# Kernel optimization log

Hardware: AMD Instinct MI355X
Metric: run time of the kernel (lower is better)

## Reference

```python
import jax, jax.numpy as jnp
import numpy as np

HIDDEN = 300
DEPTH = 3
MAX_NB = 10
AFEAT = 82
BFEAT = 6
B, N, M = 16, 2048, 4096


def setup_inputs() -> dict:
    key = jax.random.key(0)
    ks = jax.random.split(key, 16)
    s = 0.05
    return {
        "input_atom": jax.random.normal(ks[0], (B, N, AFEAT), jnp.float32),
        "input_bond": jax.random.normal(ks[1], (B, M, BFEAT), jnp.float32),
        "node_mask": jnp.ones((B, N, 1), jnp.float32),
        "atom_graph": jax.random.randint(ks[2], (B, N, MAX_NB), 0, N, jnp.int32),
        "bond_graph": jax.random.randint(ks[3], (B, N, MAX_NB), 0, M, jnp.int32),
        "num_nbs": jax.random.randint(ks[4], (B, N), 0, MAX_NB, jnp.int32),
        "W_af": jax.random.normal(ks[5], (AFEAT, HIDDEN), jnp.float32) * s,
        "W_na": jax.random.normal(ks[6], (HIDDEN, HIDDEN), jnp.float32) * s,
        "W_nb": jax.random.normal(ks[7], (BFEAT, HIDDEN), jnp.float32) * s,
        "W_sa": jax.random.normal(ks[8], (HIDDEN, HIDDEN), jnp.float32) * s,
        "W_u2": jax.random.normal(ks[9], (HIDDEN + BFEAT, HIDDEN), jnp.float32) * s,
        "b_u2": jnp.zeros((HIDDEN,), jnp.float32),
        "W_u1": jax.random.normal(ks[10], (2 * HIDDEN, HIDDEN), jnp.float32) * s,
        "b_u1": jnp.zeros((HIDDEN,), jnp.float32),
        "W_out": jax.random.normal(ks[11], (HIDDEN, 1), jnp.float32) * s,
        "b_out": jnp.zeros((1,), jnp.float32),
    }


def _wln(input_atom, input_bond, node_mask, atom_graph, bond_graph, num_nbs,
         W_af, W_na, W_nb, W_sa, W_u2, b_u2, W_u1, b_u1):
    bidx = jnp.arange(input_atom.shape[0])[:, None, None]  # (B,1,1)
    atom_feat = jax.nn.relu(input_atom @ W_af)             # (B,N,H)
    fbond_nei = input_bond[bidx, bond_graph]               # (B,N,max_nb,6) gather
    h_nei_bond = fbond_nei @ W_nb                          # constant over depth
    # neighbor validity mask from num_nbs (sequence mask)
    nb_mask = (jnp.arange(MAX_NB)[None, None, :] < num_nbs[..., None]
               ).astype(atom_feat.dtype)[..., None]        # (B,N,max_nb,1)
    kernel = None
    for _ in range(DEPTH):
        fatom_nei = atom_feat[bidx, atom_graph]            # (B,N,max_nb,H) gather
        h_nei = (fatom_nei @ W_na) * h_nei_bond
        f_nei = jnp.sum(h_nei * nb_mask, axis=-2)          # (B,N,H)
        f_self = atom_feat @ W_sa
        kernel = f_nei * f_self * node_mask                # last-layer WLN kernel
        l_nei = jnp.concatenate([fatom_nei, fbond_nei], axis=-1)
        pre_label = jax.nn.relu(l_nei @ W_u2 + b_u2)
        nei_label = jnp.sum(pre_label * nb_mask, axis=-2)
        new_label = jnp.concatenate([atom_feat, nei_label], axis=-1)
        atom_feat = jax.nn.relu(new_label @ W_u1 + b_u1)
    return kernel


def reference(input_atom, input_bond, node_mask, atom_graph, bond_graph, num_nbs,
              W_af, W_na, W_nb, W_sa, W_u2, b_u2, W_u1, b_u1, W_out, b_out):
    x = _wln(input_atom, input_bond, node_mask, atom_graph, bond_graph, num_nbs,
             W_af, W_na, W_nb, W_sa, W_u2, b_u2, W_u1, b_u1)  # (B,N,H)
    x = jnp.sum(x, axis=-2)                                   # sum pooling -> (B,H)
    return x @ W_out + b_out                                  # (B,1)
```

## Files before the change

kernel.cpp:

```cpp
#include <hip/hip_runtime.h>
#include <math.h>


typedef unsigned short ushort_t;
typedef __attribute__((ext_vector_type(8))) short bf16x8;
typedef __attribute__((ext_vector_type(8))) unsigned short ushort8;
typedef __attribute__((ext_vector_type(4))) float f32x4;

static constexpr int Hh  = 300;
static constexpr int Hp  = 320;
static constexpr int Bn  = 16;
static constexpr int Nn  = 2048;
static constexpr int Rn  = Bn * Nn;
static constexpr int NBn = 10;

__device__ __forceinline__ ushort_t f2bf(float x) {
    union { float f; unsigned u; } c; c.f = x;
    unsigned r = c.u + 0x7FFFu + ((c.u >> 16) & 1u);
    return (ushort_t)(r >> 16);
}
__device__ __forceinline__ float bf2f(ushort_t h) {
    union { float f; unsigned u; } c; c.u = ((unsigned)h) << 16;
    return c.f;
}

template<bool RELU, bool BIAS, bool CONCAT>
__global__ __launch_bounds__(256)
void mfma_gemm_k(const ushort_t* __restrict__ A, const ushort_t* __restrict__ A2,
                 int lda, int KP,
                 const ushort_t* __restrict__ Wt,
                 const float* __restrict__ bias,
                 ushort_t* __restrict__ C)
{
    __shared__ __attribute__((aligned(16))) ushort_t As[256 * 40];
    __shared__ __attribute__((aligned(16))) ushort_t Bs[64 * 40];

    const int t   = threadIdx.x;
    const int wv  = t >> 6;
    const int ln  = t & 63;
    const int lrow = ln & 15;
    const int lgrp = ln >> 4;
    const int rowBase = blockIdx.y * 256;
    const int nBase   = blockIdx.x * 64;

    f32x4 acc[4][4];
#pragma unroll
    for (int i = 0; i < 4; i++)
#pragma unroll
        for (int j = 0; j < 4; j++) acc[i][j] = (f32x4){0.f, 0.f, 0.f, 0.f};

    const int half = KP >> 1;

    for (int k0 = 0; k0 < KP; k0 += 32) {
#pragma unroll
        for (int e = 0; e < 4; e++) {
            int chunk = t + e * 256;
            int r = chunk >> 2, c = chunk & 3;
            int k = k0 + c * 8;
            const ushort_t* src;
            if (CONCAT && k >= half) src = A2 + (size_t)(rowBase + r) * lda + (k - half);
            else                     src = A  + (size_t)(rowBase + r) * lda + k;
            *(ushort8*)&As[r * 40 + c * 8] = *(const ushort8*)src;
        }
        {
            int r = t >> 2, c = t & 3;
            *(ushort8*)&Bs[r * 40 + c * 8] =
                *(const ushort8*)(Wt + (size_t)(nBase + r) * KP + k0 + c * 8);
        }
        __syncthreads();

        bf16x8 af[4], bfr[4];
#pragma unroll
        for (int mb = 0; mb < 4; mb++)
            af[mb] = *(const bf16x8*)&As[(wv * 64 + mb * 16 + lrow) * 40 + lgrp * 8];
#pragma unroll
        for (int nb = 0; nb < 4; nb++)
            bfr[nb] = *(const bf16x8*)&Bs[(nb * 16 + lrow) * 40 + lgrp * 8];
#pragma unroll
        for (int mb = 0; mb < 4; mb++)
#pragma unroll
            for (int nb = 0; nb < 4; nb++)
                acc[mb][nb] = __builtin_amdgcn_mfma_f32_16x16x32_bf16(
                    af[mb], bfr[nb], acc[mb][nb], 0, 0, 0);
        __syncthreads();
    }

#pragma unroll
    for (int mb = 0; mb < 4; mb++) {
        int row0 = rowBase + wv * 64 + mb * 16 + lgrp * 4;
#pragma unroll
        for (int nb = 0; nb < 4; nb++) {
            int col = nBase + nb * 16 + lrow;
            float bv = 0.f;
            if (BIAS) bv = (col < Hh) ? bias[col] : 0.f;
#pragma unroll
            for (int r = 0; r < 4; r++) {
                float v = acc[mb][nb][r] + bv;
                if (RELU) v = v > 0.f ? v : 0.f;
                C[(size_t)(row0 + r) * Hp + col] = f2bf(v);
            }
        }
    }
}

template<bool FINAL>
__global__ __launch_bounds__(256)
void gather_k(const ushort_t* __restrict__ Arow,
              const ushort_t* __restrict__ Asa,
              const float* __restrict__ bond,
              const float* __restrict__ Wb,
              const float* __restrict__ bias,
              const int*   __restrict__ ag,
              const int*   __restrict__ bg,
              const int*   __restrict__ nnb,
              const float* __restrict__ nmask,
              const float* __restrict__ Wout,
              void* __restrict__ outp)
{
    __shared__ float sWb[6 * Hh];
    __shared__ float sV[Hh];
    __shared__ float sdot[4];
    for (int i = threadIdx.x; i < 6 * Hh; i += 256) sWb[i] = Wb[i];
    if (FINAL) { for (int i = threadIdx.x; i < Hh; i += 256) sV[i] = Wout[i]; }
    else       { for (int i = threadIdx.x; i < Hh; i += 256) sV[i] = bias[i]; }
    __syncthreads();

    const int wave = threadIdx.x >> 6;
    const int lane = threadIdx.x & 63;
    const int node = blockIdx.x * 4 + wave;
    const int b    = node >> 11;
    const int nn   = nnb[node];
    const int base = node * NBn;

    float acc[5] = {0.f, 0.f, 0.f, 0.f, 0.f};

    for (int k = 0; k < nn; k++) {
        int ia = ag[base + k];
        int ib = bg[base + k];
        const ushort_t* pa = Arow + ((size_t)(b << 11) + ia) * Hp;
        const float*    pf = bond + ((size_t)(b << 12) + ib) * 6;
        float f0 = pf[0], f1 = pf[1], f2 = pf[2], f3 = pf[3], f4 = pf[4], f5 = pf[5];
#pragma unroll
        for (int j = 0; j < 5; j++) {
            int h = lane + j * 64;
            if (j < 4 || h < Hh) {
                float w = f0 * sWb[h]          + f1 * sWb[Hh + h]
                        + f2 * sWb[2 * Hh + h] + f3 * sWb[3 * Hh + h]
                        + f4 * sWb[4 * Hh + h] + f5 * sWb[5 * Hh + h];
                float av = bf2f(pa[h]);
                if (FINAL) {
                    acc[j] += av * w;
                } else {
                    float v = av + w + sV[h];
                    acc[j] += v > 0.f ? v : 0.f;
                }
            }
        }
    }

    if (FINAL) {
        const ushort_t* psa = Asa + (size_t)node * Hp;
        float dot = 0.f;
#pragma unroll
        for (int j = 0; j < 5; j++) {
            int h = lane + j * 64;
            if (j < 4 || h < Hh) dot += acc[j] * bf2f(psa[h]) * sV[h];
        }
        dot *= nmask[node];
#pragma unroll
        for (int off = 32; off > 0; off >>= 1) dot += __shfl_down(dot, off, 64);
        if (lane == 0) sdot[wave] = dot;
        __syncthreads();
        if (threadIdx.x == 0) {
            atomicAdd(&((float*)outp)[b], sdot[0] + sdot[1] + sdot[2] + sdot[3]);
        }
    } else {
        ushort_t* pl = (ushort_t*)outp + (size_t)node * Hp;
#pragma unroll
        for (int j = 0; j < 5; j++) {
            int h = lane + j * 64;
            if (h < Hh)      pl[h] = f2bf(acc[j]);
            else if (h < Hp) pl[h] = 0;
        }
    }
}

__global__ void zero_k(ushort_t* __restrict__ p, int n)
{
    int i = blockIdx.x * 256 + threadIdx.x;
    if (i < n) p[i] = 0;
}

__global__ void cvt_atom_k(const float* __restrict__ src, ushort_t* __restrict__ dst)
{
    int idx = blockIdx.x * 256 + threadIdx.x;
    if (idx >= Rn * 96) return;
    int r = idx / 96, c = idx - r * 96;
    dst[idx] = (c < 82) ? f2bf(src[r * 82 + c]) : (ushort_t)0;
}

__global__ void cvt_w_k(const float* __restrict__ src, ushort_t* __restrict__ dst,
                        int Ksrc, int kbase, int stride)
{
    int idx = blockIdx.x * 256 + threadIdx.x;
    if (idx >= Ksrc * Hh) return;
    int k = idx / Hh, n = idx - k * Hh;
    dst[(size_t)n * stride + kbase + k] = f2bf(src[idx]);
}

__global__ void init_out_k(float* __restrict__ out, const float* __restrict__ b_out)
{
    if (threadIdx.x < Bn) out[threadIdx.x] = b_out[0];
}

extern "C" void kernel_launch(void* const* d_in, const int* in_sizes, int n_in,
                              void* d_out, int out_size, void* d_ws, size_t ws_size,
                              hipStream_t stream)
{
    const float* input_atom = (const float*)d_in[0];
    const float* input_bond = (const float*)d_in[1];
    const float* node_mask  = (const float*)d_in[2];
    const int*   atom_graph = (const int*)d_in[3];
    const int*   bond_graph = (const int*)d_in[4];
    const int*   num_nbs    = (const int*)d_in[5];
    const float* W_af       = (const float*)d_in[6];
    const float* W_na       = (const float*)d_in[7];
    const float* W_nb       = (const float*)d_in[8];
    const float* W_sa       = (const float*)d_in[9];
    const float* W_u2       = (const float*)d_in[10];
    const float* b_u2       = (const float*)d_in[11];
    const float* W_u1       = (const float*)d_in[12];
    const float* b_u1       = (const float*)d_in[13];
    const float* W_out      = (const float*)d_in[14];
    const float* b_out      = (const float*)d_in[15];
    float* out = (float*)d_out;

    const float* W_u2b = W_u2 + (size_t)Hh * Hh;

    const size_t S2 = (size_t)Rn * Hp;
    ushort_t* bufA0 = (ushort_t*)d_ws;
    ushort_t* bufA1 = bufA0 + S2;
    ushort_t* bufP  = bufA1 + S2;
    ushort_t* bufL  = bufP  + S2;
    ushort_t* bufS  = bufL  + S2;
    ushort_t* iaB   = bufS  + S2;
    ushort_t* wAf   = iaB + (size_t)Rn * 96;
    ushort_t* wU2   = wAf + 320 * 96;
    ushort_t* wNa   = wU2 + 320 * 320;
    ushort_t* wSa   = wNa + 320 * 320;
    ushort_t* wU1   = wSa + 320 * 320;

    const int wElems = 320 * 96 + 3 * 320 * 320 + 320 * 640;
    zero_k<<<(wElems + 255) / 256, 256, 0, stream>>>(wAf, wElems);
    cvt_atom_k<<<(Rn * 96 + 255) / 256, 256, 0, stream>>>(input_atom, iaB);
    cvt_w_k<<<( 82 * 300 + 255) / 256, 256, 0, stream>>>(W_af, wAf,  82,   0,  96);
    cvt_w_k<<<(300 * 300 + 255) / 256, 256, 0, stream>>>(W_u2, wU2, 300,   0, 320);
    cvt_w_k<<<(300 * 300 + 255) / 256, 256, 0, stream>>>(W_na, wNa, 300,   0, 320);
    cvt_w_k<<<(300 * 300 + 255) / 256, 256, 0, stream>>>(W_sa, wSa, 300,   0, 320);
    cvt_w_k<<<(300 * 300 + 255) / 256, 256, 0, stream>>>(W_u1, wU1, 300,   0, 640);
    cvt_w_k<<<(300 * 300 + 255) / 256, 256, 0, stream>>>(W_u1 + 300 * 300, wU1, 300, 320, 640);
    init_out_k<<<dim3(1), dim3(64), 0, stream>>>(out, b_out);

    dim3 gg(5, Rn / 256);
    const int gb = Rn / 4;

    mfma_gemm_k<true, false, false><<<gg, 256, 0, stream>>>(
        iaB, nullptr, 96, 96, wAf, nullptr, bufA0);

    ushort_t* cur = bufA0;
    ushort_t* oth = bufA1;
    for (int d = 0; d < 2; d++) {
        mfma_gemm_k<false, false, false><<<gg, 256, 0, stream>>>(
            cur, nullptr, Hp, Hp, wU2, nullptr, bufP);
        gather_k<false><<<gb, 256, 0, stream>>>(
            bufP, nullptr, input_bond, W_u2b, b_u2,
            atom_graph, bond_graph, num_nbs, nullptr, nullptr, bufL);
        mfma_gemm_k<true, true, true><<<gg, 256, 0, stream>>>(
            cur, bufL, Hp, 2 * Hp, wU1, b_u1, oth);
        ushort_t* tmp = cur; cur = oth; oth = tmp;
    }

    mfma_gemm_k<false, false, false><<<gg, 256, 0, stream>>>(
        cur, nullptr, Hp, Hp, wNa, nullptr, bufP);
    mfma_gemm_k<false, false, false><<<gg, 256, 0, stream>>>(
        cur, nullptr, Hp, Hp, wSa, nullptr, bufS);
    gather_k<true><<<gb, 256, 0, stream>>>(
        bufP, bufS, input_bond, W_nb, nullptr,
        atom_graph, bond_graph, num_nbs, node_mask, W_out, out);
}
```

Baseline: 552.6 us.

## Software-pipeline neighbor gathers and merge weight conversion launches

```diff
diff --git a/kernel.cpp b/kernel.cpp
--- a/kernel.cpp
+++ b/kernel.cpp
@@ -13,6 +13,12 @@
 static constexpr int Nn  = 2048;
 static constexpr int Rn  = Bn * Nn;
 static constexpr int NBn = 10;
+
+static constexpr size_t OFF_U2 = 320 * 96;
+static constexpr size_t OFF_NA = OFF_U2 + 320 * 320;
+static constexpr size_t OFF_SA = OFF_NA + 320 * 320;
+static constexpr size_t OFF_U1 = OFF_SA + 320 * 320;
+static constexpr int    W_ELEMS = (int)(OFF_U1 + 320 * 640);
 
 __device__ __forceinline__ ushort_t f2bf(float x) {
     union { float f; unsigned u; } c; c.f = x;
@@ -117,37 +123,57 @@
               const float* __restrict__ Wout,
               void* __restrict__ outp)
 {
-    __shared__ float sWb[6 * Hh];
-    __shared__ float sV[Hh];
+    __shared__ float sWb[6 * Hp];
+    __shared__ float sV[Hp];
     __shared__ float sdot[4];
-    for (int i = threadIdx.x; i < 6 * Hh; i += 256) sWb[i] = Wb[i];
-    if (FINAL) { for (int i = threadIdx.x; i < Hh; i += 256) sV[i] = Wout[i]; }
-    else       { for (int i = threadIdx.x; i < Hh; i += 256) sV[i] = bias[i]; }
+    for (int i = threadIdx.x; i < 6 * Hp; i += 256) {
+        int tt = i / Hp, h = i - tt * Hp;
+        sWb[i] = (h < Hh) ? Wb[tt * Hh + h] : 0.f;
+    }
+    for (int i = threadIdx.x; i < Hp; i += 256) {
+        float v = 0.f;
+        if (i < Hh) v = FINAL ? Wout[i] : bias[i];
+        sV[i] = v;
+    }
     __syncthreads();
 
     const int wave = threadIdx.x >> 6;
     const int lane = threadIdx.x & 63;
-    const int node = blockIdx.x * 4 + wave;
-    const int b    = node >> 11;
-    const int nn   = nnb[node];
-    const int base = node * NBn;
-
-    float acc[5] = {0.f, 0.f, 0.f, 0.f, 0.f};
-
-    for (int k = 0; k < nn; k++) {
-        int ia = ag[base + k];
-        int ib = bg[base + k];
-        const ushort_t* pa = Arow + ((size_t)(b << 11) + ia) * Hp;
-        const float*    pf = bond + ((size_t)(b << 12) + ib) * 6;
-        float f0 = pf[0], f1 = pf[1], f2 = pf[2], f3 = pf[3], f4 = pf[4], f5 = pf[5];
-#pragma unroll
-        for (int j = 0; j < 5; j++) {
-            int h = lane + j * 64;
-            if (j < 4 || h < Hh) {
-                float w = f0 * sWb[h]          + f1 * sWb[Hh + h]
-                        + f2 * sWb[2 * Hh + h] + f3 * sWb[3 * Hh + h]
-                        + f4 * sWb[4 * Hh + h] + f5 * sWb[5 * Hh + h];
-                float av = bf2f(pa[h]);
+
+    int node = blockIdx.x * 4 + wave;
+
+    for (int it = 0; it < 4; it++, node += 2048 * 4) {
+        const int b    = node >> 11;
+        const int nn   = nnb[node];
+        const int base = node * NBn;
+        const size_t arow0 = (size_t)(b << 11) * Hp;
+        const size_t brow0 = (size_t)(b << 12) * 6;
+
+        const int iav = ag[base + (lane < 10 ? lane : 9)];
+        const int ibv = bg[base + (lane < 10 ? lane : 9)];
+
+        float acc[5] = {0.f, 0.f, 0.f, 0.f, 0.f};
+        float cA[6], cB[6];
+        ushort_t qA[5], qB[5];
+
+        auto issue = [&](int kk, float (&c)[6], ushort_t (&q)[5]) {
+            int iak = __shfl(iav, kk);
+            int ibk = __shfl(ibv, kk);
+            const ushort_t* pa = Arow + arow0 + (size_t)iak * Hp + lane;
+            const float*    pf = bond + brow0 + (size_t)ibk * 6;
+#pragma unroll
+            for (int j = 0; j < 5; j++) q[j] = pa[j * 64];
+#pragma unroll
+            for (int t2 = 0; t2 < 6; t2++) c[t2] = pf[t2];
+        };
+        auto consume = [&](const float (&c)[6], const ushort_t (&q)[5]) {
+#pragma unroll
+            for (int j = 0; j < 5; j++) {
+                int h = lane + j * 64;
+                float w = c[0] * sWb[h]          + c[1] * sWb[Hp + h]
+                        + c[2] * sWb[2 * Hp + h] + c[3] * sWb[3 * Hp + h]
+                        + c[4] * sWb[4 * Hp + h] + c[5] * sWb[5 * Hp + h];
+                float av = bf2f(q[j]);
                 if (FINAL) {
                     acc[j] += av * w;
                 } else {
@@ -155,32 +181,41 @@
                     acc[j] += v > 0.f ? v : 0.f;
                 }
             }
-        }
-    }
-
-    if (FINAL) {
-        const ushort_t* psa = Asa + (size_t)node * Hp;
-        float dot = 0.f;
-#pragma unroll
-        for (int j = 0; j < 5; j++) {
-            int h = lane + j * 64;
-            if (j < 4 || h < Hh) dot += acc[j] * bf2f(psa[h]) * sV[h];
-        }
-        dot *= nmask[node];
-#pragma unroll
-        for (int off = 32; off > 0; off >>= 1) dot += __shfl_down(dot, off, 64);
-        if (lane == 0) sdot[wave] = dot;
-        __syncthreads();
-        if (threadIdx.x == 0) {
-            atomicAdd(&((float*)outp)[b], sdot[0] + sdot[1] + sdot[2] + sdot[3]);
-        }
-    } else {
-        ushort_t* pl = (ushort_t*)outp + (size_t)node * Hp;
-#pragma unroll
-        for (int j = 0; j < 5; j++) {
-            int h = lane + j * 64;
-            if (h < Hh)      pl[h] = f2bf(acc[j]);
-            else if (h < Hp) pl[h] = 0;
+        };
+
+        if (nn > 0) {
+            issue(0, cA, qA);
+            if (nn > 1) issue(1, cB, qB);
+            for (int k = 0; k < nn; k += 2) {
+                consume(cA, qA);
+                if (k + 2 < nn) issue(k + 2, cA, qA);
+                if (k + 1 < nn) {
+                    consume(cB, qB);
+                    if (k + 3 < nn) issue(k + 3, cB, qB);
+                }
+            }
+        }
+
+        if (FINAL) {
+            const ushort_t* psa = Asa + (size_t)node * Hp + lane;
+            float dot = 0.f;
+#pragma unroll
+            for (int j = 0; j < 5; j++) {
+                int h = lane + j * 64;
+                dot += acc[j] * bf2f(psa[j * 64]) * sV[h];
+            }
+            dot *= nmask[node];
+#pragma unroll
+            for (int off = 32; off > 0; off >>= 1) dot += __shfl_down(dot, off, 64);
+            if (lane == 0) sdot[wave] = dot;
+            __syncthreads();
+            if (threadIdx.x == 0)
+                atomicAdd(&((float*)outp)[b], sdot[0] + sdot[1] + sdot[2] + sdot[3]);
+            __syncthreads();
+        } else {
+            ushort_t* pl = (ushort_t*)outp + (size_t)node * Hp + lane;
+#pragma unroll
+            for (int j = 0; j < 5; j++) pl[j * 64] = f2bf(acc[j]);
         }
     }
 }
@@ -199,13 +234,26 @@
     dst[idx] = (c < 82) ? f2bf(src[r * 82 + c]) : (ushort_t)0;
 }
 
-__global__ void cvt_w_k(const float* __restrict__ src, ushort_t* __restrict__ dst,
-                        int Ksrc, int kbase, int stride)
-{
+__global__ void cvt_weights_k(const float* __restrict__ W_af,
+                              const float* __restrict__ W_u2,
+                              const float* __restrict__ W_na,
+                              const float* __restrict__ W_sa,
+                              const float* __restrict__ W_u1,
+                              ushort_t* __restrict__ dst0)
+{
+    const float* src; int Ksrc, kbase, stride; size_t doff;
+    switch (blockIdx.y) {
+    case 0:  src = W_af;             Ksrc =  82; kbase = 0;   stride =  96; doff = 0;      break;
+    case 1:  src = W_u2;             Ksrc = 300; kbase = 0;   stride = 320; doff = OFF_U2; break;
+    case 2:  src = W_na;             Ksrc = 300; kbase = 0;   stride = 320; doff = OFF_NA; break;
+    case 3:  src = W_sa;             Ksrc = 300; kbase = 0;   stride = 320; doff = OFF_SA; break;
+    case 4:  src = W_u1;             Ksrc = 300; kbase = 0;   stride = 640; doff = OFF_U1; break;
+    default: src = W_u1 + 300 * 300; Ksrc = 300; kbase = 320; stride = 640; doff = OFF_U1; break;
+    }
     int idx = blockIdx.x * 256 + threadIdx.x;
     if (idx >= Ksrc * Hh) return;
     int k = idx / Hh, n = idx - k * Hh;
-    dst[(size_t)n * stride + kbase + k] = f2bf(src[idx]);
+    dst0[doff + (size_t)n * stride + kbase + k] = f2bf(src[idx]);
 }
 
 __global__ void init_out_k(float* __restrict__ out, const float* __restrict__ b_out)
@@ -245,24 +293,14 @@
     ushort_t* bufS  = bufL  + S2;
     ushort_t* iaB   = bufS  + S2;
     ushort_t* wAf   = iaB + (size_t)Rn * 96;
-    ushort_t* wU2   = wAf + 320 * 96;
-    ushort_t* wNa   = wU2 + 320 * 320;
-    ushort_t* wSa   = wNa + 320 * 320;
-    ushort_t* wU1   = wSa + 320 * 320;
-
-    const int wElems = 320 * 96 + 3 * 320 * 320 + 320 * 640;
-    zero_k<<<(wElems + 255) / 256, 256, 0, stream>>>(wAf, wElems);
+
+    zero_k<<<(W_ELEMS + 255) / 256, 256, 0, stream>>>(wAf, W_ELEMS);
     cvt_atom_k<<<(Rn * 96 + 255) / 256, 256, 0, stream>>>(input_atom, iaB);
-    cvt_w_k<<<( 82 * 300 + 255) / 256, 256, 0, stream>>>(W_af, wAf,  82,   0,  96);
-    cvt_w_k<<<(300 * 300 + 255) / 256, 256, 0, stream>>>(W_u2, wU2, 300,   0, 320);
-    cvt_w_k<<<(300 * 300 + 255) / 256, 256, 0, stream>>>(W_na, wNa, 300,   0, 320);
-    cvt_w_k<<<(300 * 300 + 255) / 256, 256, 0, stream>>>(W_sa, wSa, 300,   0, 320);
-    cvt_w_k<<<(300 * 300 + 255) / 256, 256, 0, stream>>>(W_u1, wU1, 300,   0, 640);
-    cvt_w_k<<<(300 * 300 + 255) / 256, 256, 0, stream>>>(W_u1 + 300 * 300, wU1, 300, 320, 640);
+    cvt_weights_k<<<dim3(352, 6), 256, 0, stream>>>(W_af, W_u2, W_na, W_sa, W_u1, wAf);
     init_out_k<<<dim3(1), dim3(64), 0, stream>>>(out, b_out);
 
     dim3 gg(5, Rn / 256);
-    const int gb = Rn / 4;
+    const int gb = 2048;
 
     mfma_gemm_k<true, false, false><<<gg, 256, 0, stream>>>(
         iaB, nullptr, 96, 96, wAf, nullptr, bufA0);
@@ -271,19 +309,19 @@
     ushort_t* oth = bufA1;
     for (int d = 0; d < 2; d++) {
         mfma_gemm_k<false, false, false><<<gg, 256, 0, stream>>>(
-            cur, nullptr, Hp, Hp, wU2, nullptr, bufP);
+            cur, nullptr, Hp, Hp, wAf + OFF_U2, nullptr, bufP);
         gather_k<false><<<gb, 256, 0, stream>>>(
             bufP, nullptr, input_bond, W_u2b, b_u2,
             atom_graph, bond_graph, num_nbs, nullptr, nullptr, bufL);
         mfma_gemm_k<true, true, true><<<gg, 256, 0, stream>>>(
-            cur, bufL, Hp, 2 * Hp, wU1, b_u1, oth);
+            cur, bufL, Hp, 2 * Hp, wAf + OFF_U1, b_u1, oth);
         ushort_t* tmp = cur; cur = oth; oth = tmp;
     }
 
     mfma_gemm_k<false, false, false><<<gg, 256, 0, stream>>>(
-        cur, nullptr, Hp, Hp, wNa, nullptr, bufP);
+        cur, nullptr, Hp, Hp, wAf + OFF_NA, nullptr, bufP);
     mfma_gemm_k<false, false, false><<<gg, 256, 0, stream>>>(
-        cur, nullptr, Hp, Hp, wSa, nullptr, bufS);
+        cur, nullptr, Hp, Hp, wAf + OFF_SA, nullptr, bufS);
     gather_k<true><<<gb, 256, 0, stream>>>(
         bufP, bufS, input_bond, W_nb, nullptr,
         atom_graph, bond_graph, num_nbs, node_mask, W_out, out);
```

After: 491.9 us. 1.12x faster.
